# Kernel optimization log

Hardware: AMD Instinct MI355X
Metric: run time of the kernel (lower is better)

Reference implementation:

```python
import jax, jax.numpy as jnp
import numpy as np

EMBED = 1024
HEADS = 16
HEAD = EMBED // HEADS
B, S = 8, 1024


def setup_inputs() -> dict:
    key = jax.random.key(0)
    ks = jax.random.split(key, 12)
    inp = {
        "values": jax.random.normal(ks[0], (B, S, EMBED), jnp.float32),
        "keys": jax.random.normal(ks[1], (B, S, EMBED), jnp.float32),
        "query": jax.random.normal(ks[2], (B, S, EMBED), jnp.float32),
        # causal mask broadcastable to [B, heads, q, k]
        "mask": jnp.broadcast_to(jnp.tril(jnp.ones((S, S), jnp.int32))[None, None], (B, 1, S, S)),
        "Wv": jax.random.normal(ks[3], (HEAD, HEAD), jnp.float32) / np.sqrt(HEAD),
        "bv": jnp.zeros((HEAD,), jnp.float32),
        "Wk": jax.random.normal(ks[4], (HEAD, HEAD), jnp.float32) / np.sqrt(HEAD),
        "bk": jnp.zeros((HEAD,), jnp.float32),
        "Wq": jax.random.normal(ks[5], (HEAD, HEAD), jnp.float32) / np.sqrt(HEAD),
        "bq": jnp.zeros((HEAD,), jnp.float32),
        "Wfc": jax.random.normal(ks[6], (EMBED, EMBED), jnp.float32) / np.sqrt(EMBED),
        "bfc": jnp.zeros((EMBED,), jnp.float32),
    }
    return inp


def reference(values, keys, query, mask, Wv, bv, Wk, bk, Wq, bq, Wfc, bfc):
    N, q_len = query.shape[0], query.shape[1]
    k_len, v_len = keys.shape[1], values.shape[1]
    # split heads: [N, S, H, D]
    v = values.reshape(N, v_len, HEADS, HEAD)
    k = keys.reshape(N, k_len, HEADS, HEAD)
    q = query.reshape(N, q_len, HEADS, HEAD)
    # per-head linear projections (torch Linear: x @ W.T + b)
    v = v @ Wv.T + bv
    k = k @ Wk.T + bk
    q = q @ Wq.T + bq
    # scores [N, H, q, k]
    scores = jnp.einsum('nqhz,nkhz->nhqk', q, k)
    scores = jnp.where(mask == 0, -jnp.inf, scores)
    # NOTE: original divides by sqrt(query_size) (sequence length), not head dim
    attn = jax.nn.softmax(scores / jnp.sqrt(jnp.float32(q_len)), axis=-1)
    out = jnp.einsum('nhqk,nkhz->nqhz', attn, v).reshape(N, q_len, HEADS * HEAD)
    return out @ Wfc.T + bfc
```

## Files before the change

### kernel.cpp

```cpp
#include <hip/hip_runtime.h>
#include <stdint.h>

typedef __attribute__((ext_vector_type(8))) short short8;
typedef __attribute__((ext_vector_type(4))) float floatx4;
typedef __attribute__((ext_vector_type(4))) unsigned short ushort4v;

#define HEADS 16
#define HEAD 64
#define SEQ 1024
#define BATCH 8

__device__ __forceinline__ unsigned short f2bf(float f) {
    union { float f; unsigned int u; } v; v.f = f;
    unsigned int r = v.u + 0x7FFFu + ((v.u >> 16) & 1u);
    return (unsigned short)(r >> 16);
}

__device__ __forceinline__ void gload_lds16(const void* g, void* l) {
    __builtin_amdgcn_global_load_lds((const __attribute__((address_space(1))) void*)g,
                                     (__attribute__((address_space(3))) void*)l, 16, 0, 0);
}

__global__ __launch_bounds__(256) void proj_qk_kernel(
    const float* __restrict__ Qin, const float* __restrict__ Kin,
    const float* __restrict__ Wq, const float* __restrict__ bq,
    const float* __restrict__ Wk, const float* __restrict__ bk,
    unsigned short* __restrict__ q_ws, unsigned short* __restrict__ k_ws)
{
    const int tid = threadIdx.x;
    const int wave = tid >> 6, lane = tid & 63;
    const int lq = lane & 15, quad = lane >> 4;
    const int proj = blockIdx.y;

    const float* X = proj ? Kin : Qin;
    const float* W = proj ? Wk : Wq;
    const float* bias = proj ? bk : bq;
    unsigned short* dstb = proj ? k_ws : q_ws;

    const int gr0 = blockIdx.x * 16;
    const int h0 = wave * 4;
    const int b = gr0 >> 10, s0 = gr0 & 1023;

    __shared__ unsigned short sT[4][16 * 68];

    short8 wf[4][2];
#pragma unroll
    for (int nt = 0; nt < 4; ++nt) {
        const float* wr = W + (nt * 16 + lq) * 64 + quad * 8;
#pragma unroll
        for (int ks = 0; ks < 2; ++ks) {
            float4 f0 = *(const float4*)(wr + ks * 32);
            float4 f1 = *(const float4*)(wr + ks * 32 + 4);
            short8 v;
            v[0] = (short)f2bf(f0.x); v[1] = (short)f2bf(f0.y);
            v[2] = (short)f2bf(f0.z); v[3] = (short)f2bf(f0.w);
            v[4] = (short)f2bf(f1.x); v[5] = (short)f2bf(f1.y);
            v[6] = (short)f2bf(f1.z); v[7] = (short)f2bf(f1.w);
            wf[nt][ks] = v;
        }
    }

    float bqk[4];
#pragma unroll
    for (int nt = 0; nt < 4; ++nt) bqk[nt] = bias[nt * 16 + lq];
    const float qscale = 0.03125f * 1.44269504088896340736f;
    const float oscale = proj ? 1.0f : qscale;

    const float* xb = X + (size_t)(gr0 + lq) * 1024 + quad * 8;
    const floatx4 zero4 = {0.f, 0.f, 0.f, 0.f};

    unsigned short* tw = &sT[wave][0];
    const unsigned short* tr = &sT[wave][(lane >> 2) * 68 + (lane & 3) * 16];

    float4 xf[4];
    { const float* p = xb + h0 * 64;
      xf[0] = *(const float4*)p;        xf[1] = *(const float4*)(p + 4);
      xf[2] = *(const float4*)(p + 32); xf[3] = *(const float4*)(p + 36); }
#pragma unroll
    for (int hh = 0; hh < 4; ++hh) {
        float4 xn[4];
        if (hh < 3) {
            const float* p = xb + (h0 + hh + 1) * 64;
            xn[0] = *(const float4*)p;        xn[1] = *(const float4*)(p + 4);
            xn[2] = *(const float4*)(p + 32); xn[3] = *(const float4*)(p + 36);
        }
        short8 aq[2];
#pragma unroll
        for (int ks = 0; ks < 2; ++ks) {
            short8 a;
            a[0] = (short)f2bf(xf[ks * 2].x);     a[1] = (short)f2bf(xf[ks * 2].y);
            a[2] = (short)f2bf(xf[ks * 2].z);     a[3] = (short)f2bf(xf[ks * 2].w);
            a[4] = (short)f2bf(xf[ks * 2 + 1].x); a[5] = (short)f2bf(xf[ks * 2 + 1].y);
            a[6] = (short)f2bf(xf[ks * 2 + 1].z); a[7] = (short)f2bf(xf[ks * 2 + 1].w);
            aq[ks] = a;
        }
        floatx4 acc[4] = {zero4, zero4, zero4, zero4};
#pragma unroll
        for (int ks = 0; ks < 2; ++ks)
#pragma unroll
            for (int nt = 0; nt < 4; ++nt)
                acc[nt] = __builtin_amdgcn_mfma_f32_16x16x32_bf16(aq[ks], wf[nt][ks], acc[nt], 0, 0, 0);

#pragma unroll
        for (int nt = 0; nt < 4; ++nt)
#pragma unroll
            for (int r = 0; r < 4; ++r)
                tw[(quad * 4 + r) * 68 + nt * 16 + lq] = f2bf((acc[nt][r] + bqk[nt]) * oscale);

        short8 o0 = *(const short8*)tr;
        short8 o1 = *(const short8*)(tr + 8);
        unsigned short* dst = dstb + ((size_t)((b * 16 + h0 + hh) * 1024) + s0) * 64 + lane * 16;
        *(short8*)dst = o0;
        *(short8*)(dst + 8) = o1;

#pragma unroll
        for (int i = 0; i < 4; ++i) xf[i] = xn[i];
    }
}

__global__ __launch_bounds__(256) void proj_v_kernel(
    const float* __restrict__ Vin,
    const float* __restrict__ Wv, const float* __restrict__ bv,
    const float* __restrict__ Wfc, unsigned short* __restrict__ wfc_ws,
    unsigned short* __restrict__ v_ws)
{
    const int tid = threadIdx.x;
    const int wave = tid >> 6, lane = tid & 63;
    const int lq = lane & 15, quad = lane >> 4;

    {
        int base = blockIdx.x * 2048 + tid * 8;
        float4 f0 = *(const float4*)(Wfc + base);
        float4 f1 = *(const float4*)(Wfc + base + 4);
        ushort4v v0, v1;
        v0.x = f2bf(f0.x); v0.y = f2bf(f0.y); v0.z = f2bf(f0.z); v0.w = f2bf(f0.w);
        v1.x = f2bf(f1.x); v1.y = f2bf(f1.y); v1.z = f2bf(f1.z); v1.w = f2bf(f1.w);
        *(ushort4v*)(wfc_ws + base) = v0;
        *(ushort4v*)(wfc_ws + base + 4) = v1;
    }

    const int gr0 = blockIdx.x * 16;
    const int h0 = wave * 4;
    const int b = gr0 >> 10, s0 = gr0 & 1023;

    __shared__ unsigned short sT[4][64 * 20];

    short8 wf[4][2];
#pragma unroll
    for (int nt = 0; nt < 4; ++nt) {
        const float* wr = Wv + (nt * 16 + lq) * 64 + quad * 8;
#pragma unroll
        for (int ks = 0; ks < 2; ++ks) {
            float4 f0 = *(const float4*)(wr + ks * 32);
            float4 f1 = *(const float4*)(wr + ks * 32 + 4);
            short8 v;
            v[0] = (short)f2bf(f0.x); v[1] = (short)f2bf(f0.y);
            v[2] = (short)f2bf(f0.z); v[3] = (short)f2bf(f0.w);
            v[4] = (short)f2bf(f1.x); v[5] = (short)f2bf(f1.y);
            v[6] = (short)f2bf(f1.z); v[7] = (short)f2bf(f1.w);
            wf[nt][ks] = v;
        }
    }

    float bvr[4][4];
#pragma unroll
    for (int nt = 0; nt < 4; ++nt)
#pragma unroll
        for (int r = 0; r < 4; ++r) bvr[nt][r] = bv[nt * 16 + quad * 4 + r];

    const float* xb = Vin + (size_t)(gr0 + lq) * 1024 + quad * 8;
    const floatx4 zero4 = {0.f, 0.f, 0.f, 0.f};

    unsigned short* tw = &sT[wave][0];
    const int rrow = lane >> 1, rhalf = lane & 1;
    const unsigned short* tr0 = &sT[wave][rrow * 20 + rhalf * 8];
    const unsigned short* tr1 = &sT[wave][(rrow + 32) * 20 + rhalf * 8];

    float4 xf[4];
    { const float* p = xb + h0 * 64;
      xf[0] = *(const float4*)p;        xf[1] = *(const float4*)(p + 4);
      xf[2] = *(const float4*)(p + 32); xf[3] = *(const float4*)(p + 36); }
#pragma unroll
    for (int hh = 0; hh < 4; ++hh) {
        float4 xn[4];
        if (hh < 3) {
            const float* p = xb + (h0 + hh + 1) * 64;
            xn[0] = *(const float4*)p;        xn[1] = *(const float4*)(p + 4);
            xn[2] = *(const float4*)(p + 32); xn[3] = *(const float4*)(p + 36);
        }
        short8 aq[2];
#pragma unroll
        for (int ks = 0; ks < 2; ++ks) {
            short8 a;
            a[0] = (short)f2bf(xf[ks * 2].x);     a[1] = (short)f2bf(xf[ks * 2].y);
            a[2] = (short)f2bf(xf[ks * 2].z);     a[3] = (short)f2bf(xf[ks * 2].w);
            a[4] = (short)f2bf(xf[ks * 2 + 1].x); a[5] = (short)f2bf(xf[ks * 2 + 1].y);
            a[6] = (short)f2bf(xf[ks * 2 + 1].z); a[7] = (short)f2bf(xf[ks * 2 + 1].w);
            aq[ks] = a;
        }
        floatx4 acc[4] = {zero4, zero4, zero4, zero4};
#pragma unroll
        for (int ks = 0; ks < 2; ++ks)
#pragma unroll
            for (int nt = 0; nt < 4; ++nt)
                acc[nt] = __builtin_amdgcn_mfma_f32_16x16x32_bf16(wf[nt][ks], aq[ks], acc[nt], 0, 0, 0);

#pragma unroll
        for (int nt = 0; nt < 4; ++nt)
#pragma unroll
            for (int r = 0; r < 4; ++r)
                tw[(nt * 16 + quad * 4 + r) * 20 + lq] = f2bf(acc[nt][r] + bvr[nt][r]);

        short8 o0 = *(const short8*)tr0;
        short8 o1 = *(const short8*)tr1;
        unsigned short* vh = v_ws + (size_t)((b * 16 + h0 + hh) * 64) * 1024 + s0 + rhalf * 8;
        *(short8*)(vh + (size_t)rrow * 1024) = o0;
        *(short8*)(vh + (size_t)(rrow + 32) * 1024) = o1;

#pragma unroll
        for (int i = 0; i < 4; ++i) xf[i] = xn[i];
    }
}

__global__ __launch_bounds__(256, 4) void attn_kernel(
    const unsigned short* __restrict__ q_ws, const unsigned short* __restrict__ k_ws,
    const unsigned short* __restrict__ v_ws, unsigned short* __restrict__ attn_ws)
{
    const int bh = blockIdx.x;
    const int b = bh >> 4, h = bh & 15;
    const int tid = threadIdx.x;
    const int wave = tid >> 6, lane = tid & 63;
    const int lq = lane & 15, quad = lane >> 4;
    const int r8 = lane >> 3, ch = lane & 7;
    const int sw = ch ^ r8;

    __shared__ unsigned short sK[64 * 64];
    __shared__ unsigned short sV[64 * 64];
    __shared__ unsigned short sP[4][32 * 64];

    const size_t head_off = (size_t)bh * SEQ * HEAD;
    const unsigned short* qb = q_ws + head_off;
    const unsigned short* kb = k_ws + head_off;
    const unsigned short* vb = v_ws + head_off;

    short8 ones;
#pragma unroll
    for (int j = 0; j < 8; ++j) ones[j] = (short)0x3F80;

    const floatx4 zero4 = {0.f, 0.f, 0.f, 0.f};

    const int qt = blockIdx.y;
    const int q0 = qt * 128;
    const int q_lo = q0 + wave * 32;
    const int q_hi = q_lo + 31;
    const int nkt = 2 * qt + 2;

    short8 aq[2][2];
#pragma unroll
    for (int rg = 0; rg < 2; ++rg) {
        const unsigned short* qp = qb + (size_t)(q0 + wave * 32 + rg * 16 + lq) * 64 + quad * 8;
        aq[rg][0] = *(const short8*)qp;
        aq[rg][1] = *(const short8*)(qp + 32);
    }

    floatx4 o[2][4];
    floatx4 lacc[2] = {zero4, zero4};
#pragma unroll
    for (int rg = 0; rg < 2; ++rg)
#pragma unroll
        for (int nt = 0; nt < 4; ++nt) o[rg][nt] = zero4;

    for (int kt = 0; kt < nkt; ++kt) {
#pragma unroll
        for (int i = 0; i < 2; ++i) {
            int br = wave * 16 + i * 8;
            const char* gK = (const char*)(kb + (size_t)(kt * 64 + br + r8) * 64) + sw * 16;
            gload_lds16(gK, (char*)sK + br * 128);
            const char* gV = (const char*)(vb + (size_t)(br + r8) * 1024 + kt * 64) + sw * 16;
            gload_lds16(gV, (char*)sV + br * 128);
        }
        __syncthreads();

        const bool skip = (kt * 64 > q_hi);
        if (!skip) {
            const bool full = (kt * 64 + 63 <= q_lo);

            floatx4 s[2][4];
#pragma unroll
            for (int rg = 0; rg < 2; ++rg)
#pragma unroll
                for (int nt = 0; nt < 4; ++nt) s[rg][nt] = zero4;
#pragma unroll
            for (int ks = 0; ks < 2; ++ks) {
#pragma unroll
                for (int nt = 0; nt < 4; ++nt) {
                    short8 kf = *(const short8*)(sK + (nt * 16 + lq) * 64 +
                                                 (((quad + 4 * ks) ^ (lq & 7)) * 8));
                    s[0][nt] = __builtin_amdgcn_mfma_f32_16x16x32_bf16(aq[0][ks], kf, s[0][nt], 0, 0, 0);
                    s[1][nt] = __builtin_amdgcn_mfma_f32_16x16x32_bf16(aq[1][ks], kf, s[1][nt], 0, 0, 0);
                }
            }

            unsigned short* wp = &sP[wave][0];
#pragma unroll
            for (int rg = 0; rg < 2; ++rg) {
#pragma unroll
                for (int nt = 0; nt < 4; ++nt) {
                    int kcol = kt * 64 + nt * 16 + lq;
                    int chn = (((nt * 2 + (lq >> 3)) ^ (quad << 1)) * 8) + (lq & 7);
#pragma unroll
                    for (int r = 0; r < 4; ++r) {
                        float p = __builtin_amdgcn_exp2f(s[rg][nt][r]);
                        if (!full) {
                            int qrow = q_lo + rg * 16 + quad * 4 + r;
                            if (kcol > qrow) p = 0.f;
                        }
                        wp[(rg * 16 + quad * 4 + r) * 64 + chn] = f2bf(p);
                    }
                }
            }

            short8 vf[4][2];
#pragma unroll
            for (int nt = 0; nt < 4; ++nt)
#pragma unroll
                for (int ks = 0; ks < 2; ++ks)
                    vf[nt][ks] = *(const short8*)(sV + (nt * 16 + lq) * 64 +
                                                  (((quad + 4 * ks) ^ (lq & 7)) * 8));
#pragma unroll
            for (int rg = 0; rg < 2; ++rg) {
#pragma unroll
                for (int ks = 0; ks < 2; ++ks) {
                    short8 pa = *(const short8*)&sP[wave][(rg * 16 + lq) * 64 +
                                 (((ks * 4 + quad) ^ (((lq >> 2) & 3) << 1)) * 8)];
                    lacc[rg] = __builtin_amdgcn_mfma_f32_16x16x32_bf16(pa, ones, lacc[rg], 0, 0, 0);
#pragma unroll
                    for (int nt = 0; nt < 4; ++nt)
                        o[rg][nt] = __builtin_amdgcn_mfma_f32_16x16x32_bf16(pa, vf[nt][ks], o[rg][nt], 0, 0, 0);
                }
            }
        }
        __syncthreads();
    }

#pragma unroll
    for (int rg = 0; rg < 2; ++rg) {
        float inv[4];
#pragma unroll
        for (int r = 0; r < 4; ++r) inv[r] = 1.f / lacc[rg][r];
        const int srow_base = q0 + wave * 32 + rg * 16 + quad * 4;
#pragma unroll
        for (int nt = 0; nt < 4; ++nt) {
            int col = h * 64 + nt * 16 + lq;
#pragma unroll
            for (int r = 0; r < 4; ++r) {
                attn_ws[((size_t)(b * SEQ + srow_base + r)) * 1024 + col] = f2bf(o[rg][nt][r] * inv[r]);
            }
        }
    }
}

__global__ __launch_bounds__(256) void fc_kernel(
    const unsigned short* __restrict__ A, const unsigned short* __restrict__ Bw,
    const float* __restrict__ bias, float* __restrict__ out)
{
    const int nt0 = blockIdx.x * 128;
    const int mt0 = blockIdx.y * 128;
    const int tid = threadIdx.x;
    const int wave = tid >> 6, lane = tid & 63;
    const int lq = lane & 15, quad = lane >> 4;
    const int wm = (wave >> 1) * 64, wn = (wave & 1) * 64;

    __shared__ unsigned short sA[128 * 64];
    __shared__ unsigned short sB[128 * 64];

    const floatx4 zero4 = {0.f, 0.f, 0.f, 0.f};
    floatx4 acc[4][4];
#pragma unroll
    for (int i = 0; i < 4; ++i)
#pragma unroll
        for (int j = 0; j < 4; ++j) acc[i][j] = zero4;

    const int sc = (tid & 7) ^ ((tid >> 3) & 7);
    const int sr = tid >> 3;

    for (int kt = 0; kt < 16; ++kt) {
#pragma unroll
        for (int j = 0; j < 4; ++j) {
            int r = j * 32 + sr;
            const char* ga = (const char*)A + (size_t)(mt0 + r) * 2048 + kt * 128 + sc * 16;
            gload_lds16(ga, (char*)sA + (j * 256 + tid) * 16);
            const char* gb = (const char*)Bw + (size_t)(nt0 + r) * 2048 + kt * 128 + sc * 16;
            gload_lds16(gb, (char*)sB + (j * 256 + tid) * 16);
        }
        __syncthreads();

        short8 af[4][2], bf[4][2];
#pragma unroll
        for (int i = 0; i < 4; ++i)
#pragma unroll
            for (int ks = 0; ks < 2; ++ks) {
                af[i][ks] = *(const short8*)(sA + (wm + i * 16 + lq) * 64 +
                                             (((quad + 4 * ks) ^ (lq & 7)) * 8));
                bf[i][ks] = *(const short8*)(sB + (wn + i * 16 + lq) * 64 +
                                             (((quad + 4 * ks) ^ (lq & 7)) * 8));
            }
#pragma unroll
        for (int ks = 0; ks < 2; ++ks)
#pragma unroll
            for (int mi = 0; mi < 4; ++mi)
#pragma unroll
                for (int ni = 0; ni < 4; ++ni)
                    acc[mi][ni] = __builtin_amdgcn_mfma_f32_16x16x32_bf16(af[mi][ks], bf[ni][ks], acc[mi][ni], 0, 0, 0);
        __syncthreads();
    }

#pragma unroll
    for (int mi = 0; mi < 4; ++mi) {
#pragma unroll
        for (int ni = 0; ni < 4; ++ni) {
            int col = nt0 + wn + ni * 16 + lq;
            float bc = bias[col];
#pragma unroll
            for (int r = 0; r < 4; ++r) {
                int row = mt0 + wm + mi * 16 + quad * 4 + r;
                out[(size_t)row * 1024 + col] = acc[mi][ni][r] + bc;
            }
        }
    }
}

extern "C" void kernel_launch(void* const* d_in, const int* in_sizes, int n_in,
                              void* d_out, int out_size, void* d_ws, size_t ws_size,
                              hipStream_t stream)
{
    const float* values = (const float*)d_in[0];
    const float* keys   = (const float*)d_in[1];
    const float* query  = (const float*)d_in[2];
    const float* Wv  = (const float*)d_in[4];
    const float* bv  = (const float*)d_in[5];
    const float* Wk  = (const float*)d_in[6];
    const float* bk  = (const float*)d_in[7];
    const float* Wq  = (const float*)d_in[8];
    const float* bq  = (const float*)d_in[9];
    const float* Wfc = (const float*)d_in[10];
    const float* bfc = (const float*)d_in[11];
    float* out = (float*)d_out;

    char* ws = (char*)d_ws;
    unsigned short* q_ws    = (unsigned short*)(ws);
    unsigned short* k_ws    = (unsigned short*)(ws + (16u << 20));
    unsigned short* v_ws    = (unsigned short*)(ws + (32u << 20));
    unsigned short* attn_ws = (unsigned short*)(ws + (48u << 20));
    unsigned short* wfc_ws  = (unsigned short*)(ws + (64u << 20));

    proj_qk_kernel<<<dim3(512, 2), dim3(256), 0, stream>>>(
        query, keys, Wq, bq, Wk, bk, q_ws, k_ws);
    proj_v_kernel<<<dim3(512), dim3(256), 0, stream>>>(values, Wv, bv, Wfc, wfc_ws, v_ws);
    attn_kernel<<<dim3(128, 8), dim3(256), 0, stream>>>(q_ws, k_ws, v_ws, attn_ws);
    fc_kernel<<<dim3(8, 64), dim3(256), 0, stream>>>(attn_ws, wfc_ws, bfc, out);
}
```

Before: 256.8 us.

## Balance causal attention work by pairing mirrored 64-row query tiles per block

The attention kernel now splits each 128-row query tile into two 64-row passes. Each block handles query tile t and its mirror 15-t, so every block processes the same number of key/value tiles under the causal mask instead of workload growing with blockIdx.y. Each wave now owns 16 query rows instead of 32, which shrinks register and LDS use. The cost is more K/V tile traffic per query row and less reuse of each K/V fragment across rows within a wave.

```diff
diff --git a/kernel.cpp b/kernel.cpp
--- a/kernel.cpp
+++ b/kernel.cpp
@@ -236,7 +236,7 @@
 
     __shared__ unsigned short sK[64 * 64];
     __shared__ unsigned short sV[64 * 64];
-    __shared__ unsigned short sP[4][32 * 64];
+    __shared__ unsigned short sP[4][16 * 64];
 
     const size_t head_off = (size_t)bh * SEQ * HEAD;
     const unsigned short* qb = q_ws + head_off;
@@ -249,74 +249,62 @@
 
     const floatx4 zero4 = {0.f, 0.f, 0.f, 0.f};
 
-    const int qt = blockIdx.y;
-    const int q0 = qt * 128;
-    const int q_lo = q0 + wave * 32;
-    const int q_hi = q_lo + 31;
-    const int nkt = 2 * qt + 2;
-
-    short8 aq[2][2];
-#pragma unroll
-    for (int rg = 0; rg < 2; ++rg) {
-        const unsigned short* qp = qb + (size_t)(q0 + wave * 32 + rg * 16 + lq) * 64 + quad * 8;
-        aq[rg][0] = *(const short8*)qp;
-        aq[rg][1] = *(const short8*)(qp + 32);
-    }
-
-    floatx4 o[2][4];
-    floatx4 lacc[2] = {zero4, zero4};
-#pragma unroll
-    for (int rg = 0; rg < 2; ++rg)
-#pragma unroll
-        for (int nt = 0; nt < 4; ++nt) o[rg][nt] = zero4;
-
-    for (int kt = 0; kt < nkt; ++kt) {
-#pragma unroll
-        for (int i = 0; i < 2; ++i) {
-            int br = wave * 16 + i * 8;
-            const char* gK = (const char*)(kb + (size_t)(kt * 64 + br + r8) * 64) + sw * 16;
-            gload_lds16(gK, (char*)sK + br * 128);
-            const char* gV = (const char*)(vb + (size_t)(br + r8) * 1024 + kt * 64) + sw * 16;
-            gload_lds16(gV, (char*)sV + br * 128);
-        }
-        __syncthreads();
-
-        const bool skip = (kt * 64 > q_hi);
-        if (!skip) {
-            const bool full = (kt * 64 + 63 <= q_lo);
-
-            floatx4 s[2][4];
-#pragma unroll
-            for (int rg = 0; rg < 2; ++rg)
-#pragma unroll
-                for (int nt = 0; nt < 4; ++nt) s[rg][nt] = zero4;
+    for (int pass = 0; pass < 2; ++pass) {
+        const int t = pass ? (15 - blockIdx.y) : blockIdx.y;
+        const int q0 = t * 64;
+        const int nkt = t + 1;
+
+        short8 aq[2];
+        {
+            const unsigned short* qp = qb + (size_t)(q0 + wave * 16 + lq) * 64 + quad * 8;
+            aq[0] = *(const short8*)qp;
+            aq[1] = *(const short8*)(qp + 32);
+        }
+
+        floatx4 o[4];
+        floatx4 lacc = zero4;
+#pragma unroll
+        for (int nt = 0; nt < 4; ++nt) o[nt] = zero4;
+
+        for (int kt = 0; kt < nkt; ++kt) {
+#pragma unroll
+            for (int i = 0; i < 2; ++i) {
+                int br = wave * 16 + i * 8;
+                const char* gK = (const char*)(kb + (size_t)(kt * 64 + br + r8) * 64) + sw * 16;
+                gload_lds16(gK, (char*)sK + br * 128);
+                const char* gV = (const char*)(vb + (size_t)(br + r8) * 1024 + kt * 64) + sw * 16;
+                gload_lds16(gV, (char*)sV + br * 128);
+            }
+            __syncthreads();
+
+            const bool full = (kt != t);
+
+            floatx4 s[4];
+#pragma unroll
+            for (int nt = 0; nt < 4; ++nt) s[nt] = zero4;
 #pragma unroll
             for (int ks = 0; ks < 2; ++ks) {
 #pragma unroll
                 for (int nt = 0; nt < 4; ++nt) {
                     short8 kf = *(const short8*)(sK + (nt * 16 + lq) * 64 +
                                                  (((quad + 4 * ks) ^ (lq & 7)) * 8));
-                    s[0][nt] = __builtin_amdgcn_mfma_f32_16x16x32_bf16(aq[0][ks], kf, s[0][nt], 0, 0, 0);
-                    s[1][nt] = __builtin_amdgcn_mfma_f32_16x16x32_bf16(aq[1][ks], kf, s[1][nt], 0, 0, 0);
+                    s[nt] = __builtin_amdgcn_mfma_f32_16x16x32_bf16(aq[ks], kf, s[nt], 0, 0, 0);
                 }
             }
 
             unsigned short* wp = &sP[wave][0];
 #pragma unroll
-            for (int rg = 0; rg < 2; ++rg) {
-#pragma unroll
-                for (int nt = 0; nt < 4; ++nt) {
-                    int kcol = kt * 64 + nt * 16 + lq;
-                    int chn = (((nt * 2 + (lq >> 3)) ^ (quad << 1)) * 8) + (lq & 7);
-#pragma unroll
-                    for (int r = 0; r < 4; ++r) {
-                        float p = __builtin_amdgcn_exp2f(s[rg][nt][r]);
-                        if (!full) {
-                            int qrow = q_lo + rg * 16 + quad * 4 + r;
-                            if (kcol > qrow) p = 0.f;
-                        }
-                        wp[(rg * 16 + quad * 4 + r) * 64 + chn] = f2bf(p);
+            for (int nt = 0; nt < 4; ++nt) {
+                int kcol = nt * 16 + lq;
+                int chn = (((nt * 2 + (lq >> 3)) ^ (quad << 1)) * 8) + (lq & 7);
+#pragma unroll
+                for (int r = 0; r < 4; ++r) {
+                    float p = __builtin_amdgcn_exp2f(s[nt][r]);
+                    if (!full) {
+                        int qrow = wave * 16 + quad * 4 + r;
+                        if (kcol > qrow) p = 0.f;
                     }
+                    wp[(quad * 4 + r) * 64 + chn] = f2bf(p);
                 }
             }
 
@@ -328,33 +316,27 @@
                     vf[nt][ks] = *(const short8*)(sV + (nt * 16 + lq) * 64 +
                                                   (((quad + 4 * ks) ^ (lq & 7)) * 8));
 #pragma unroll
-            for (int rg = 0; rg < 2; ++rg) {
-#pragma unroll
-                for (int ks = 0; ks < 2; ++ks) {
-                    short8 pa = *(const short8*)&sP[wave][(rg * 16 + lq) * 64 +
-                                 (((ks * 4 + quad) ^ (((lq >> 2) & 3) << 1)) * 8)];
-                    lacc[rg] = __builtin_amdgcn_mfma_f32_16x16x32_bf16(pa, ones, lacc[rg], 0, 0, 0);
-#pragma unroll
-                    for (int nt = 0; nt < 4; ++nt)
-                        o[rg][nt] = __builtin_amdgcn_mfma_f32_16x16x32_bf16(pa, vf[nt][ks], o[rg][nt], 0, 0, 0);
-                }
-            }
-        }
-        __syncthreads();
-    }
-
-#pragma unroll
-    for (int rg = 0; rg < 2; ++rg) {
+            for (int ks = 0; ks < 2; ++ks) {
+                short8 pa = *(const short8*)&sP[wave][lq * 64 +
+                             (((ks * 4 + quad) ^ (((lq >> 2) & 3) << 1)) * 8)];
+                lacc = __builtin_amdgcn_mfma_f32_16x16x32_bf16(pa, ones, lacc, 0, 0, 0);
+#pragma unroll
+                for (int nt = 0; nt < 4; ++nt)
+                    o[nt] = __builtin_amdgcn_mfma_f32_16x16x32_bf16(pa, vf[nt][ks], o[nt], 0, 0, 0);
+            }
+            __syncthreads();
+        }
+
         float inv[4];
 #pragma unroll
-        for (int r = 0; r < 4; ++r) inv[r] = 1.f / lacc[rg][r];
-        const int srow_base = q0 + wave * 32 + rg * 16 + quad * 4;
+        for (int r = 0; r < 4; ++r) inv[r] = 1.f / lacc[r];
+        const int srow_base = q0 + wave * 16 + quad * 4;
 #pragma unroll
         for (int nt = 0; nt < 4; ++nt) {
             int col = h * 64 + nt * 16 + lq;
 #pragma unroll
             for (int r = 0; r < 4; ++r) {
-                attn_ws[((size_t)(b * SEQ + srow_base + r)) * 1024 + col] = f2bf(o[rg][nt][r] * inv[r]);
+                attn_ws[((size_t)(b * SEQ + srow_base + r)) * 1024 + col] = f2bf(o[nt][r] * inv[r]);
             }
         }
     }
```

After: 252.9 us. No clear change (-1.5%).
